# Performance work log

Hardware: AMD Instinct MI355X
Metric: run time of the kernel (lower is better)

The kernel has to match this reference:

```python
import jax, jax.numpy as jnp
import numpy as np

N_EMBD = 1024
HEAD_SIZE = 64

def setup_inputs() -> dict:
    key = jax.random.key(0)
    k1, k2, k3, k4 = jax.random.split(key, 4)
    x = jax.random.normal(k1, (8, 2048, N_EMBD), dtype=jnp.float32)
    s = 1.0 / np.sqrt(N_EMBD)
    Wk = jax.random.normal(k2, (HEAD_SIZE, N_EMBD), dtype=jnp.float32) * s
    Wq = jax.random.normal(k3, (HEAD_SIZE, N_EMBD), dtype=jnp.float32) * s
    Wv = jax.random.normal(k4, (HEAD_SIZE, N_EMBD), dtype=jnp.float32) * s
    return {"x": x, "Wk": Wk, "Wq": Wq, "Wv": Wv}

def reference(x, Wk, Wq, Wv):
    B, T, C = x.shape
    k = jnp.einsum('btc,hc->bth', x, Wk)  # [B,T,Hd]
    q = jnp.einsum('btc,hc->bth', x, Wq)
    v = jnp.einsum('btc,hc->bth', x, Wv)
    # NOTE: original scales by C**-0.5 where C = n_embd (not head_size)
    wei = jnp.einsum('bqh,bkh->bqk', q, k) * (C ** -0.5)  # [B,T,T]
    causal = jnp.tril(jnp.ones((T, T), dtype=bool))
    wei = jnp.where(causal, wei, -jnp.inf)
    wei = jax.nn.softmax(wei, axis=-1)
    out = jnp.einsum('bqk,bkh->bqh', wei, v)  # [B,T,Hd]
    return out
```

## Files before the change

### kernel.cpp

```cpp
#include <hip/hip_runtime.h>


typedef __attribute__((ext_vector_type(4))) short sv4;
typedef __attribute__((ext_vector_type(8))) short sv8;
typedef __attribute__((ext_vector_type(4))) float f32x4;

#define NB   8
#define TSEQ 2048
#define CDIM 1024
#define HD   64
#define MROWS (NB * TSEQ)

__device__ __forceinline__ short f2s(float f) {
  union { float f; unsigned u; } v; v.f = f;
  unsigned u = v.u;
  u += 0x7fffu + ((u >> 16) & 1u);
  return (short)(u >> 16);
}
__device__ __forceinline__ unsigned pk2(float lo, float hi) {
  return (unsigned)(unsigned short)f2s(lo) | ((unsigned)(unsigned short)f2s(hi) << 16);
}
__device__ __forceinline__ void glds16(const short* g, short* l) {
  __builtin_amdgcn_global_load_lds(
      (const __attribute__((address_space(1))) unsigned int*)g,
      (__attribute__((address_space(3))) unsigned int*)l, 16, 0, 0);
}

__global__ __launch_bounds__(256) void wcvt(
    const float* __restrict__ Wq, const float* __restrict__ Wk,
    const float* __restrict__ Wv, short* __restrict__ wb)
{
  int i = blockIdx.x * 256 + threadIdx.x;
  int t = i / 1536;
  int rem = i - t * 1536;
  int r = rem >> 3, s = rem & 7;
  int j = r >> 6, wrow = r & 63;
  const float* W = (j == 0) ? Wq : (j == 1) ? Wk : Wv;
  const float* src = W + (size_t)wrow * CDIM + t * 64 + ((s ^ (wrow & 7)) << 3);
  float4 a = *(const float4*)src;
  float4 b = *(const float4*)(src + 4);
  sv8 v = {f2s(a.x), f2s(a.y), f2s(a.z), f2s(a.w),
           f2s(b.x), f2s(b.y), f2s(b.z), f2s(b.w)};
  *(sv8*)(wb + (size_t)i * 8) = v;
}

__global__ __launch_bounds__(1024) void qkv_proj(
    const float* __restrict__ x,
    const short* __restrict__ wb,
    short* __restrict__ qw,
    short* __restrict__ kw,
    short* __restrict__ vtw)
{
  __shared__ short wlds[2][12288];
  __shared__ short xlds[2][4096];
  const int tid  = threadIdx.x;
  const int wid  = tid >> 6;
  const int lane = tid & 63;
  const int g    = lane >> 4;
  const int c16  = lane & 15;
  const int rowg = wid >> 2;
  const int ph   = wid & 3;
  const int row0 = blockIdx.x * 64;

  const int xr = tid >> 4, xs = tid & 15;
  const float* xsrc = x + (size_t)(row0 + xr) * CDIM + xs * 4;
  const int xwo = xr * 64 + (((xs >> 1) ^ (xr & 7)) << 3) + (xs & 1) * 4;

  const int arow = rowg * 16 + c16;
  const int x7   = c16 & 7;
  int rWo[3];
  #pragma unroll
  for (int p6 = 0; p6 < 3; ++p6) {
    int p = ph * 3 + p6;
    rWo[p6] = ((p >> 2) * 64 + (p & 3) * 16 + c16) * 64;
  }

  f32x4 acc[3];
  #pragma unroll
  for (int p6 = 0; p6 < 3; ++p6) acc[p6] = (f32x4){0.f, 0.f, 0.f, 0.f};

  float4 px[3];

  glds16(wb + (size_t)tid * 8, &wlds[0][tid * 8]);
  if (wid < 8) glds16(wb + (size_t)(1024 + tid) * 8, &wlds[0][(1024 + tid) * 8]);
  px[0] = *(const float4*)(xsrc);
  px[1] = *(const float4*)(xsrc + 64);
  px[2] = *(const float4*)(xsrc + 128);
  asm volatile("s_waitcnt vmcnt(2)" ::: "memory");
  {
    sv4 v = {f2s(px[0].x), f2s(px[0].y), f2s(px[0].z), f2s(px[0].w)};
    *(sv4*)&xlds[0][xwo] = v;
  }
  asm volatile("s_waitcnt lgkmcnt(0)" ::: "memory");
  __builtin_amdgcn_sched_barrier(0);
  __builtin_amdgcn_s_barrier();

  #pragma unroll
  for (int t = 0; t < 16; ++t) {
    const int buf = t & 1;
    if (t < 15) {
      glds16(wb + (size_t)(t + 1) * 12288 + tid * 8, &wlds[buf ^ 1][tid * 8]);
      if (wid < 8)
        glds16(wb + (size_t)(t + 1) * 12288 + (1024 + tid) * 8,
               &wlds[buf ^ 1][(1024 + tid) * 8]);
    }
    if (t < 13) px[t % 3] = *(const float4*)(xsrc + (t + 3) * 64);
    if (t < 15) {
      float4 f = px[(t + 1) % 3];
      sv4 v = {f2s(f.x), f2s(f.y), f2s(f.z), f2s(f.w)};
      *(sv4*)&xlds[buf ^ 1][xwo] = v;
    }
    #pragma unroll
    for (int kk = 0; kk < 2; ++kk) {
      int so = ((kk * 4 + g) ^ x7) << 3;
      sv8 a = *(const sv8*)&xlds[buf][arow * 64 + so];
      #pragma unroll
      for (int p6 = 0; p6 < 3; ++p6) {
        sv8 bfr = *(const sv8*)&wlds[buf][rWo[p6] + so];
        acc[p6] = __builtin_amdgcn_mfma_f32_16x16x32_bf16(a, bfr, acc[p6], 0, 0, 0);
      }
    }
    if (t < 15) {
      if (t < 13) asm volatile("s_waitcnt vmcnt(1) lgkmcnt(0)" ::: "memory");
      else        asm volatile("s_waitcnt vmcnt(0) lgkmcnt(0)" ::: "memory");
      __builtin_amdgcn_sched_barrier(0);
      __builtin_amdgcn_s_barrier();
    }
  }

  #pragma unroll
  for (int p6 = 0; p6 < 3; ++p6) {
    int p = ph * 3 + p6, j = p >> 2, n = p & 3;
    #pragma unroll
    for (int r = 0; r < 4; ++r) {
      int rr = row0 + rowg * 16 + (g << 2) + r;
      int cc = (n << 4) + c16;
      if (j == 0) {
        qw[(size_t)rr * HD + cc] = f2s(acc[p6][r] * 0.03125f);
      } else if (j == 1) {
        kw[(size_t)rr * HD + ((((cc >> 3) ^ (rr & 7)) << 3) | (cc & 7))] =
            f2s(acc[p6][r]);
      } else {
        int b = rr >> 11, ti = rr & (TSEQ - 1);
        int kt = ti >> 6, key = ti & 63;
        vtw[(((size_t)b * 32 + kt) * 64 + cc) * 64 +
            ((((key >> 3) ^ (cc & 7)) << 3) | (key & 7))] = f2s(acc[p6][r]);
      }
    }
  }
}

__global__ __launch_bounds__(256) void attn(
    const short* __restrict__ qw,
    const short* __restrict__ kw,
    const short* __restrict__ vtw,
    float* __restrict__ Opart,
    float* __restrict__ mlws)
{
  __shared__ short kbuf[2][4096];
  __shared__ short vbuf[2][4096];
  __shared__ short bridge[4][1024];

  const int tid  = threadIdx.x;
  const int wid  = tid >> 6;
  const int lane = tid & 63;
  const int g    = lane >> 4;
  const int c16  = lane & 15;

  const int bid   = blockIdx.x;
  const int h     = bid >> 8;
  const int sub   = bid & 255;
  const int batch = sub & 7;
  const int jj    = sub >> 3;
  const int qb    = h ? (31 - jj) : jj;
  const int q0    = qb << 6;
  const size_t base = (size_t)batch * TSEQ * HD;

  const int ntot = qb + 1;
  const int th_  = (ntot + 1) >> 1;
  const int t0   = h ? th_ : 0;
  const int t1   = h ? ntot : th_;

  const int qrow = q0 + (wid << 4) + c16;
  sv8 qa0 = *(const sv8*)(qw + base + (size_t)qrow * HD + (g << 3));
  sv8 qa1 = *(const sv8*)(qw + base + (size_t)qrow * HD + 32 + (g << 3));

  float m = -1e30f, l = 0.f;
  f32x4 o[4];
  #pragma unroll
  for (int n = 0; n < 4; ++n) o[n] = (f32x4){0.f, 0.f, 0.f, 0.f};

  short* br = &bridge[wid][0];
  const int sx = c16 & 7;

  #define STAGE(tt, bb)                                                      \
    {                                                                        \
      const short* ksrc = kw + base + (size_t)(tt) * 4096;                   \
      const short* vsrc = vtw + ((size_t)batch * 32 + (tt)) * 4096;          \
      glds16(ksrc + tid * 8,         &kbuf[bb][tid * 8]);                    \
      glds16(ksrc + (256 + tid) * 8, &kbuf[bb][(256 + tid) * 8]);            \
      glds16(vsrc + tid * 8,         &vbuf[bb][tid * 8]);                    \
      glds16(vsrc + (256 + tid) * 8, &vbuf[bb][(256 + tid) * 8]);            \
    }

  if (t0 < t1) {
    STAGE(t0, 0);
    asm volatile("s_waitcnt vmcnt(0)" ::: "memory");
    __builtin_amdgcn_s_barrier();

    for (int t = t0; t < t1; ++t) {
      const int buf = (t - t0) & 1;
      if (t + 1 < t1) STAGE(t + 1, buf ^ 1);

      f32x4 s[4];
      #pragma unroll
      for (int n = 0; n < 4; ++n) s[n] = (f32x4){0.f, 0.f, 0.f, 0.f};
      #pragma unroll
      for (int n = 0; n < 4; ++n) {
        int kr = (n << 4) + c16;
        sv8 k0 = *(const sv8*)&kbuf[buf][kr * 64 + ((g ^ (kr & 7)) << 3)];
        s[n] = __builtin_amdgcn_mfma_f32_16x16x32_bf16(k0, qa0, s[n], 0, 0, 0);
        sv8 k1 = *(const sv8*)&kbuf[buf][kr * 64 + (((4 + g) ^ (kr & 7)) << 3)];
        s[n] = __builtin_amdgcn_mfma_f32_16x16x32_bf16(k1, qa1, s[n], 0, 0, 0);
      }

      if (t == qb) {
        #pragma unroll
        for (int n = 0; n < 4; ++n) {
          int key = (t << 6) + (n << 4) + (g << 2);
          #pragma unroll
          for (int r = 0; r < 4; ++r)
            s[n][r] = (key + r <= qrow) ? s[n][r] : -1e30f;
        }
      }

      float mx = -1e30f;
      #pragma unroll
      for (int n = 0; n < 4; ++n)
        mx = fmaxf(mx, fmaxf(fmaxf(s[n][0], s[n][1]), fmaxf(s[n][2], s[n][3])));
      mx = fmaxf(mx, __shfl_xor(mx, 16));
      mx = fmaxf(mx, __shfl_xor(mx, 32));
      float mnew  = fmaxf(m, mx);
      float alpha = __expf(m - mnew);
      m = mnew;

      float sum = 0.f;
      #pragma unroll
      for (int n = 0; n < 4; ++n) {
        float p0 = __expf(s[n][0] - mnew);
        float p1 = __expf(s[n][1] - mnew);
        float p2 = __expf(s[n][2] - mnew);
        float p3 = __expf(s[n][3] - mnew);
        sum += (p0 + p1) + (p2 + p3);
        int slot = 2 * n + (g >> 1);
        uint2 w2; w2.x = pk2(p0, p1); w2.y = pk2(p2, p3);
        *(uint2*)&br[c16 * 64 + ((slot ^ sx) << 3) + (g & 1) * 4] = w2;
      }
      sum += __shfl_xor(sum, 16);
      sum += __shfl_xor(sum, 32);
      l = l * alpha + sum;

      float af[4];
      #pragma unroll
      for (int r = 0; r < 4; ++r) af[r] = __shfl(alpha, (g << 2) + r);
      #pragma unroll
      for (int n = 0; n < 4; ++n)
        #pragma unroll
        for (int r = 0; r < 4; ++r) o[n][r] *= af[r];

      asm volatile("s_waitcnt lgkmcnt(0)" ::: "memory");
      __builtin_amdgcn_sched_barrier(0);

      #pragma unroll
      for (int kk = 0; kk < 2; ++kk) {
        sv8 pa = *(const sv8*)&br[c16 * 64 + ((((kk << 2) + g) ^ sx) << 3)];
        #pragma unroll
        for (int n = 0; n < 4; ++n) {
          int vr = (n << 4) + c16;
          sv8 vf = *(const sv8*)&vbuf[buf][vr * 64 +
                                           ((((kk << 2) + g) ^ (vr & 7)) << 3)];
          o[n] = __builtin_amdgcn_mfma_f32_16x16x32_bf16(pa, vf, o[n], 0, 0, 0);
        }
      }

      if (t + 1 < t1) {
        asm volatile("s_waitcnt vmcnt(0)" ::: "memory");
        __builtin_amdgcn_sched_barrier(0);
        __builtin_amdgcn_s_barrier();
      }
    }
  }

  #pragma unroll
  for (int n = 0; n < 4; ++n) {
    #pragma unroll
    for (int r = 0; r < 4; ++r) {
      int row = (wid << 4) + (g << 2) + r;
      Opart[(size_t)bid * 4096 + row * 64 + (n << 4) + c16] = o[n][r];
    }
  }
  if (lane < 16) {
    int row = (wid << 4) + lane;
    mlws[((size_t)bid * 64 + row) * 2]     = m;
    mlws[((size_t)bid * 64 + row) * 2 + 1] = l;
  }
  #undef STAGE
}

__global__ __launch_bounds__(256) void combine(
    const float* __restrict__ Opart,
    const float* __restrict__ mlws,
    float* __restrict__ out)
{
  const int bid   = blockIdx.x;
  const int batch = bid & 7;
  const int qb    = bid >> 3;
  const int q0    = qb << 6;
  const int bid0  = bid;
  const int bid1  = 256 + ((31 - qb) << 3) + batch;

  const int tid = threadIdx.x;
  const int row = tid >> 2;
  const int cs  = (tid & 3) << 4;

  float m0 = mlws[((size_t)bid0 * 64 + row) * 2];
  float l0 = mlws[((size_t)bid0 * 64 + row) * 2 + 1];
  float m1 = mlws[((size_t)bid1 * 64 + row) * 2];
  float l1 = mlws[((size_t)bid1 * 64 + row) * 2 + 1];
  float M  = fmaxf(m0, m1);
  float a0 = __expf(m0 - M), a1 = __expf(m1 - M);
  float invL = 1.f / (l0 * a0 + l1 * a1);

  const float* O0 = Opart + (size_t)bid0 * 4096 + row * 64 + cs;
  const float* O1 = Opart + (size_t)bid1 * 4096 + row * 64 + cs;
  float* op = out + ((size_t)batch * TSEQ + q0 + row) * HD + cs;

  #pragma unroll
  for (int e = 0; e < 4; ++e) {
    float4 v0 = *(const float4*)(O0 + e * 4);
    float4 v1 = *(const float4*)(O1 + e * 4);
    float4 res;
    res.x = (v0.x * a0 + v1.x * a1) * invL;
    res.y = (v0.y * a0 + v1.y * a1) * invL;
    res.z = (v0.z * a0 + v1.z * a1) * invL;
    res.w = (v0.w * a0 + v1.w * a1) * invL;
    *(float4*)(op + e * 4) = res;
  }
}

extern "C" void kernel_launch(void* const* d_in, const int* in_sizes, int n_in,
                              void* d_out, int out_size, void* d_ws, size_t ws_size,
                              hipStream_t stream) {
  const float* x  = (const float*)d_in[0];
  const float* Wk = (const float*)d_in[1];
  const float* Wq = (const float*)d_in[2];
  const float* Wv = (const float*)d_in[3];
  float* out = (float*)d_out;

  short* qw  = (short*)d_ws;
  short* kw  = qw + (size_t)MROWS * HD;
  short* vtw = kw + (size_t)MROWS * HD;
  short* wb  = vtw + (size_t)NB * HD * TSEQ;
  float* Opart = (float*)(wb + 24576 * 8);
  float* mlws  = Opart + (size_t)512 * 4096;

  wcvt<<<dim3(96), dim3(256), 0, stream>>>(Wq, Wk, Wv, wb);
  qkv_proj<<<dim3(MROWS / 64), dim3(1024), 0, stream>>>(x, wb, qw, kw, vtw);
  attn<<<dim3(512), dim3(256), 0, stream>>>(qw, kw, vtw, Opart, mlws);
  combine<<<dim3(256), dim3(256), 0, stream>>>(Opart, mlws, out);
}
```

Measured before the change: 57.69 us.

## Double K-tile depth in projection and key-tile width in attention

The QKV projection now processes 128-wide K chunks per stage (8 iterations instead of 16), with weight packing and LDS layouts reswizzled to match. Attention now consumes 128 keys per tile, with doubled K/V/bridge LDS buffers, 8 score MFMA groups and masking on the halved tile index. s_setprio is raised around the MFMA blocks. The goal is fewer barriers and loop iterations per unit of work, at the cost of more LDS per block and possibly lower occupancy. Causal work on the diagonal tile becomes coarser, so more masked keys are computed.

```diff
diff --git a/kernel.cpp b/kernel.cpp
--- a/kernel.cpp
+++ b/kernel.cpp
@@ -31,12 +31,12 @@
     const float* __restrict__ Wv, short* __restrict__ wb)
 {
   int i = blockIdx.x * 256 + threadIdx.x;
-  int t = i / 1536;
-  int rem = i - t * 1536;
-  int r = rem >> 3, s = rem & 7;
+  int t = i / 3072;
+  int rem = i - t * 3072;
+  int r = rem >> 4, s = rem & 15;
   int j = r >> 6, wrow = r & 63;
   const float* W = (j == 0) ? Wq : (j == 1) ? Wk : Wv;
-  const float* src = W + (size_t)wrow * CDIM + t * 64 + ((s ^ (wrow & 7)) << 3);
+  const float* src = W + (size_t)wrow * CDIM + t * 128 + ((s ^ (wrow & 7)) << 3);
   float4 a = *(const float4*)src;
   float4 b = *(const float4*)(src + 4);
   sv8 v = {f2s(a.x), f2s(a.y), f2s(a.z), f2s(a.w),
@@ -51,8 +51,8 @@
     short* __restrict__ kw,
     short* __restrict__ vtw)
 {
-  __shared__ short wlds[2][12288];
-  __shared__ short xlds[2][4096];
+  __shared__ short wlds[2][24576];
+  __shared__ short xlds[2][8192];
   const int tid  = threadIdx.x;
   const int wid  = tid >> 6;
   const int lane = tid & 63;
@@ -63,66 +63,76 @@
   const int row0 = blockIdx.x * 64;
 
   const int xr = tid >> 4, xs = tid & 15;
-  const float* xsrc = x + (size_t)(row0 + xr) * CDIM + xs * 4;
-  const int xwo = xr * 64 + (((xs >> 1) ^ (xr & 7)) << 3) + (xs & 1) * 4;
+  const float* xsrc = x + (size_t)(row0 + xr) * CDIM + xs * 8;
+  const int xwo = xr * 128 + ((xs ^ (xr & 7)) << 3);
 
   const int arow = rowg * 16 + c16;
-  const int x7   = c16 & 7;
-  int rWo[3];
+  const int x7   = arow & 7;
+  int rWo[3], rW7[3];
   #pragma unroll
   for (int p6 = 0; p6 < 3; ++p6) {
     int p = ph * 3 + p6;
-    rWo[p6] = ((p >> 2) * 64 + (p & 3) * 16 + c16) * 64;
+    int r = (p >> 2) * 64 + (p & 3) * 16 + c16;
+    rWo[p6] = r * 128;
+    rW7[p6] = r & 7;
   }
 
   f32x4 acc[3];
   #pragma unroll
   for (int p6 = 0; p6 < 3; ++p6) acc[p6] = (f32x4){0.f, 0.f, 0.f, 0.f};
 
-  float4 px[3];
-
-  glds16(wb + (size_t)tid * 8, &wlds[0][tid * 8]);
-  if (wid < 8) glds16(wb + (size_t)(1024 + tid) * 8, &wlds[0][(1024 + tid) * 8]);
-  px[0] = *(const float4*)(xsrc);
-  px[1] = *(const float4*)(xsrc + 64);
-  px[2] = *(const float4*)(xsrc + 128);
+  float4 px[2][2];
+
+  #pragma unroll
+  for (int k2 = 0; k2 < 3; ++k2)
+    glds16(wb + (size_t)(tid + k2 * 1024) * 8, &wlds[0][(tid + k2 * 1024) * 8]);
+  px[0][0] = *(const float4*)(xsrc);
+  px[0][1] = *(const float4*)(xsrc + 4);
+  px[1][0] = *(const float4*)(xsrc + 128);
+  px[1][1] = *(const float4*)(xsrc + 132);
   asm volatile("s_waitcnt vmcnt(2)" ::: "memory");
   {
-    sv4 v = {f2s(px[0].x), f2s(px[0].y), f2s(px[0].z), f2s(px[0].w)};
-    *(sv4*)&xlds[0][xwo] = v;
+    float4 A = px[0][0], B = px[0][1];
+    sv8 v = {f2s(A.x), f2s(A.y), f2s(A.z), f2s(A.w),
+             f2s(B.x), f2s(B.y), f2s(B.z), f2s(B.w)};
+    *(sv8*)&xlds[0][xwo] = v;
   }
   asm volatile("s_waitcnt lgkmcnt(0)" ::: "memory");
   __builtin_amdgcn_sched_barrier(0);
   __builtin_amdgcn_s_barrier();
 
   #pragma unroll
-  for (int t = 0; t < 16; ++t) {
+  for (int t = 0; t < 8; ++t) {
     const int buf = t & 1;
-    if (t < 15) {
-      glds16(wb + (size_t)(t + 1) * 12288 + tid * 8, &wlds[buf ^ 1][tid * 8]);
-      if (wid < 8)
-        glds16(wb + (size_t)(t + 1) * 12288 + (1024 + tid) * 8,
-               &wlds[buf ^ 1][(1024 + tid) * 8]);
-    }
-    if (t < 13) px[t % 3] = *(const float4*)(xsrc + (t + 3) * 64);
-    if (t < 15) {
-      float4 f = px[(t + 1) % 3];
-      sv4 v = {f2s(f.x), f2s(f.y), f2s(f.z), f2s(f.w)};
-      *(sv4*)&xlds[buf ^ 1][xwo] = v;
+    if (t < 7) {
+      #pragma unroll
+      for (int k2 = 0; k2 < 3; ++k2)
+        glds16(wb + (size_t)((t + 1) * 3072 + tid + k2 * 1024) * 8,
+               &wlds[buf ^ 1][(tid + k2 * 1024) * 8]);
+    }
+    if (t < 6) {
+      px[t & 1][0] = *(const float4*)(xsrc + (t + 2) * 128);
+      px[t & 1][1] = *(const float4*)(xsrc + (t + 2) * 128 + 4);
+    }
+    if (t < 7) {
+      float4 A = px[(t + 1) & 1][0], B = px[(t + 1) & 1][1];
+      sv8 v = {f2s(A.x), f2s(A.y), f2s(A.z), f2s(A.w),
+               f2s(B.x), f2s(B.y), f2s(B.z), f2s(B.w)};
+      *(sv8*)&xlds[buf ^ 1][xwo] = v;
     }
     #pragma unroll
-    for (int kk = 0; kk < 2; ++kk) {
-      int so = ((kk * 4 + g) ^ x7) << 3;
-      sv8 a = *(const sv8*)&xlds[buf][arow * 64 + so];
+    for (int kk = 0; kk < 4; ++kk) {
+      int kslot = kk * 4 + g;
+      sv8 a = *(const sv8*)&xlds[buf][arow * 128 + ((kslot ^ x7) << 3)];
       #pragma unroll
       for (int p6 = 0; p6 < 3; ++p6) {
-        sv8 bfr = *(const sv8*)&wlds[buf][rWo[p6] + so];
+        sv8 bfr = *(const sv8*)&wlds[buf][rWo[p6] + ((kslot ^ rW7[p6]) << 3)];
         acc[p6] = __builtin_amdgcn_mfma_f32_16x16x32_bf16(a, bfr, acc[p6], 0, 0, 0);
       }
     }
-    if (t < 15) {
-      if (t < 13) asm volatile("s_waitcnt vmcnt(1) lgkmcnt(0)" ::: "memory");
-      else        asm volatile("s_waitcnt vmcnt(0) lgkmcnt(0)" ::: "memory");
+    if (t < 7) {
+      if (t < 6) asm volatile("s_waitcnt vmcnt(2) lgkmcnt(0)" ::: "memory");
+      else       asm volatile("s_waitcnt vmcnt(0) lgkmcnt(0)" ::: "memory");
       __builtin_amdgcn_sched_barrier(0);
       __builtin_amdgcn_s_barrier();
     }
@@ -157,9 +167,9 @@
     float* __restrict__ Opart,
     float* __restrict__ mlws)
 {
-  __shared__ short kbuf[2][4096];
-  __shared__ short vbuf[2][4096];
-  __shared__ short bridge[4][1024];
+  __shared__ short kbuf[2][8192];
+  __shared__ short vbuf[2][8192];
+  __shared__ short bridge[4][2048];
 
   const int tid  = threadIdx.x;
   const int wid  = tid >> 6;
@@ -176,7 +186,7 @@
   const int q0    = qb << 6;
   const size_t base = (size_t)batch * TSEQ * HD;
 
-  const int ntot = qb + 1;
+  const int ntot = (qb >> 1) + 1;
   const int th_  = (ntot + 1) >> 1;
   const int t0   = h ? th_ : 0;
   const int t1   = h ? ntot : th_;
@@ -191,16 +201,18 @@
   for (int n = 0; n < 4; ++n) o[n] = (f32x4){0.f, 0.f, 0.f, 0.f};
 
   short* br = &bridge[wid][0];
-  const int sx = c16 & 7;
+  const int sx = c16 & 15;
 
   #define STAGE(tt, bb)                                                      \
     {                                                                        \
-      const short* ksrc = kw + base + (size_t)(tt) * 4096;                   \
-      const short* vsrc = vtw + ((size_t)batch * 32 + (tt)) * 4096;          \
-      glds16(ksrc + tid * 8,         &kbuf[bb][tid * 8]);                    \
-      glds16(ksrc + (256 + tid) * 8, &kbuf[bb][(256 + tid) * 8]);            \
-      glds16(vsrc + tid * 8,         &vbuf[bb][tid * 8]);                    \
-      glds16(vsrc + (256 + tid) * 8, &vbuf[bb][(256 + tid) * 8]);            \
+      const short* ksrc = kw + base + (size_t)(tt) * 8192;                   \
+      const short* vsrc = vtw + ((size_t)batch * 32 + (tt) * 2) * 4096;      \
+      _Pragma("unroll")                                                      \
+      for (int q = 0; q < 4; ++q)                                            \
+        glds16(ksrc + (tid + q * 256) * 8, &kbuf[bb][(tid + q * 256) * 8]);  \
+      _Pragma("unroll")                                                      \
+      for (int q = 0; q < 4; ++q)                                            \
+        glds16(vsrc + (tid + q * 256) * 8, &vbuf[bb][(tid + q * 256) * 8]);  \
     }
 
   if (t0 < t1) {
@@ -212,22 +224,24 @@
       const int buf = (t - t0) & 1;
       if (t + 1 < t1) STAGE(t + 1, buf ^ 1);
 
-      f32x4 s[4];
-      #pragma unroll
-      for (int n = 0; n < 4; ++n) s[n] = (f32x4){0.f, 0.f, 0.f, 0.f};
-      #pragma unroll
-      for (int n = 0; n < 4; ++n) {
+      f32x4 s[8];
+      #pragma unroll
+      for (int n = 0; n < 8; ++n) s[n] = (f32x4){0.f, 0.f, 0.f, 0.f};
+      __builtin_amdgcn_s_setprio(1);
+      #pragma unroll
+      for (int n = 0; n < 8; ++n) {
         int kr = (n << 4) + c16;
         sv8 k0 = *(const sv8*)&kbuf[buf][kr * 64 + ((g ^ (kr & 7)) << 3)];
         s[n] = __builtin_amdgcn_mfma_f32_16x16x32_bf16(k0, qa0, s[n], 0, 0, 0);
         sv8 k1 = *(const sv8*)&kbuf[buf][kr * 64 + (((4 + g) ^ (kr & 7)) << 3)];
         s[n] = __builtin_amdgcn_mfma_f32_16x16x32_bf16(k1, qa1, s[n], 0, 0, 0);
       }
-
-      if (t == qb) {
+      __builtin_amdgcn_s_setprio(0);
+
+      if (t == (qb >> 1)) {
         #pragma unroll
-        for (int n = 0; n < 4; ++n) {
-          int key = (t << 6) + (n << 4) + (g << 2);
+        for (int n = 0; n < 8; ++n) {
+          int key = (t << 7) + (n << 4) + (g << 2);
           #pragma unroll
           for (int r = 0; r < 4; ++r)
             s[n][r] = (key + r <= qrow) ? s[n][r] : -1e30f;
@@ -236,7 +250,7 @@
 
       float mx = -1e30f;
       #pragma unroll
-      for (int n = 0; n < 4; ++n)
+      for (int n = 0; n < 8; ++n)
         mx = fmaxf(mx, fmaxf(fmaxf(s[n][0], s[n][1]), fmaxf(s[n][2], s[n][3])));
       mx = fmaxf(mx, __shfl_xor(mx, 16));
       mx = fmaxf(mx, __shfl_xor(mx, 32));
@@ -246,7 +260,7 @@
 
       float sum = 0.f;
       #pragma unroll
-      for (int n = 0; n < 4; ++n) {
+      for (int n = 0; n < 8; ++n) {
         float p0 = __expf(s[n][0] - mnew);
         float p1 = __expf(s[n][1] - mnew);
         float p2 = __expf(s[n][2] - mnew);
@@ -254,7 +268,7 @@
         sum += (p0 + p1) + (p2 + p3);
         int slot = 2 * n + (g >> 1);
         uint2 w2; w2.x = pk2(p0, p1); w2.y = pk2(p2, p3);
-        *(uint2*)&br[c16 * 64 + ((slot ^ sx) << 3) + (g & 1) * 4] = w2;
+        *(uint2*)&br[c16 * 128 + ((slot ^ sx) << 3) + ((g & 1) << 2)] = w2;
       }
       sum += __shfl_xor(sum, 16);
       sum += __shfl_xor(sum, 32);
@@ -271,17 +285,20 @@
       asm volatile("s_waitcnt lgkmcnt(0)" ::: "memory");
       __builtin_amdgcn_sched_barrier(0);
 
-      #pragma unroll
-      for (int kk = 0; kk < 2; ++kk) {
-        sv8 pa = *(const sv8*)&br[c16 * 64 + ((((kk << 2) + g) ^ sx) << 3)];
+      __builtin_amdgcn_s_setprio(1);
+      #pragma unroll
+      for (int kk = 0; kk < 4; ++kk) {
+        int kslot = (kk << 2) + g;
+        sv8 pa = *(const sv8*)&br[c16 * 128 + ((kslot ^ sx) << 3)];
         #pragma unroll
         for (int n = 0; n < 4; ++n) {
           int vr = (n << 4) + c16;
-          sv8 vf = *(const sv8*)&vbuf[buf][vr * 64 +
-                                           ((((kk << 2) + g) ^ (vr & 7)) << 3)];
+          sv8 vf = *(const sv8*)&vbuf[buf][(kslot >> 3) * 4096 + vr * 64 +
+                                           (((kslot & 7) ^ (vr & 7)) << 3)];
           o[n] = __builtin_amdgcn_mfma_f32_16x16x32_bf16(pa, vf, o[n], 0, 0, 0);
         }
       }
+      __builtin_amdgcn_s_setprio(0);
 
       if (t + 1 < t1) {
         asm volatile("s_waitcnt vmcnt(0)" ::: "memory");
```

After: 51.62 us. -10.5%, faster.
